# Performance work log

Hardware: AMD Instinct MI355X
Metric: run time of the kernel (lower is better)

## Reference

```python
import jax, jax.numpy as jnp
import numpy as np
import math

H = 16
D_MODEL = 1024
D_K = D_MODEL // H  # 64
B = 4
S = 2048
D_V = 64


def setup_inputs() -> dict:
    key0 = jax.random.key(0)
    ks = jax.random.split(key0, 7)
    scale = 1.0 / math.sqrt(D_MODEL)
    return {
        "query": jax.random.normal(ks[0], (B, S, D_MODEL), jnp.float32),
        "key": jax.random.normal(ks[1], (B, S, D_MODEL), jnp.float32),
        "value": jax.random.normal(ks[2], (B, D_V, S), jnp.float32),
        "Wq": jax.random.normal(ks[3], (D_MODEL, D_MODEL), jnp.float32) * scale,
        "bq": jax.random.normal(ks[4], (D_MODEL,), jnp.float32) * scale,
        "Wk": jax.random.normal(ks[5], (D_MODEL, D_MODEL), jnp.float32) * scale,
        "bk": jax.random.normal(ks[6], (D_MODEL,), jnp.float32) * scale,
    }


def reference(query, key, value, Wq, bq, Wk, bk):
    nb = query.shape[0]
    # Linear projections then split heads: [B,S,d_model] -> [B,h,S,d_k]
    q = (query @ Wq.T + bq).reshape(nb, -1, H, D_K).transpose(0, 2, 1, 3)
    k = (key @ Wk.T + bk).reshape(nb, -1, H, D_K).transpose(0, 2, 1, 3)
    # value.repeat(h,1,1,1).permute(1,0,3,2): [B,dv,Sk] -> broadcast over heads
    # with last two axes swapped -> effectively v[b,s,d] = value[b,d,s]
    v = jnp.swapaxes(value, 1, 2)  # [B, Sk, dv]
    # Scaled dot-product attention (mask branch is a no-op: m == zeros)
    scores = jnp.einsum("bhqd,bhkd->bhqk", q, k) / math.sqrt(D_K)
    p_attn = jax.nn.softmax(scores, axis=-1)
    # value identical across heads, contract directly with base v
    x = jnp.einsum("bhqk,bkd->bhqd", p_attn, v)  # [B,h,Sq,dv]
    return (jnp.mean(x, axis=1), q)
```

## Files before the change

### kernel.cpp

```cpp
#include <hip/hip_runtime.h>


typedef unsigned short u16;
typedef __attribute__((ext_vector_type(8))) u16 u16x8;
typedef __attribute__((ext_vector_type(8))) __bf16 bf16x8;
typedef __attribute__((ext_vector_type(4))) float f32x4;
typedef __attribute__((ext_vector_type(16))) float f32x16;
typedef __attribute__((ext_vector_type(2))) unsigned u32x2;
typedef __attribute__((ext_vector_type(4))) unsigned u32x4;

typedef const __attribute__((address_space(1))) void gvoid;
typedef __attribute__((address_space(3))) void lvoid;

__device__ __forceinline__ void gload16(const void* g, void* l) {
  __builtin_amdgcn_global_load_lds((gvoid*)g, (lvoid*)l, 16, 0, 0);
}

__device__ __forceinline__ u16 f2bf(float f) {
  unsigned u = __builtin_bit_cast(unsigned, f);
  u += 0x7fffu + ((u >> 16) & 1u);
  return (u16)(u >> 16);
}

__device__ __forceinline__ unsigned cvtpk(float lo, float hi) {
  unsigned r;
  asm("v_cvt_pk_bf16_f32 %0, %1, %2" : "=v"(r) : "v"(lo), "v"(hi));
  return r;
}

__device__ __forceinline__ float exp2a(float x) {
  float r;
  asm("v_exp_f32 %0, %1" : "=v"(r) : "v"(x));
  return r;
}

__device__ __forceinline__ f32x16 zero16() {
  f32x16 z;
#pragma unroll
  for (int i = 0; i < 16; ++i) z[i] = 0.f;
  return z;
}

__global__ void cvt_small(const float* __restrict__ wq, const float* __restrict__ wk,
                          const float* __restrict__ v,
                          u16* __restrict__ wqb, u16* __restrict__ wkb, u16* __restrict__ vb) {
  int i = blockIdx.x * 256 + threadIdx.x;
  const float* s;
  u16* d;
  int off;
  if (i < 262144)      { s = wq; d = wqb; off = i; }
  else if (i < 524288) { s = wk; d = wkb; off = i - 262144; }
  else if (i < 655360) { s = v;  d = vb;  off = i - 524288; }
  else return;
  float4 x = reinterpret_cast<const float4*>(s)[off];
  ushort4 o;
  o.x = f2bf(x.x); o.y = f2bf(x.y); o.z = f2bf(x.z); o.w = f2bf(x.w);
  reinterpret_cast<ushort4*>(d)[off] = o;
}

__global__ __launch_bounds__(256) void proj_gemm(
    const float* __restrict__ qf, const float* __restrict__ kf,
    const u16* __restrict__ Wqb, const u16* __restrict__ Wkb,
    const float* __restrict__ bq, const float* __restrict__ bk,
    float* __restrict__ out1, u16* __restrict__ k_ws)
{
  const int z = blockIdx.z;
  const float* __restrict__ A = z ? kf : qf;
  const u16* __restrict__ W = z ? Wkb : Wqb;
  const float* __restrict__ bias = z ? bk : bq;

  __shared__ u16 As[128 * 64];
  __shared__ u16 Bs[128 * 64];

  const int tid = threadIdx.x;
  const int lane = tid & 63;
  const int w = tid >> 6;
  const int ln = lane & 15;
  const int lh = lane >> 4;
  const int wm = w >> 1, wn = w & 1;
  const int n0 = blockIdx.x * 128;
  const int j0 = blockIdx.y * 128;

  f32x4 acc[4][4];
#pragma unroll
  for (int mt = 0; mt < 4; ++mt)
#pragma unroll
    for (int nt = 0; nt < 4; ++nt)
      acc[mt][nt] = f32x4{0.f, 0.f, 0.f, 0.f};

  const int r_ = tid >> 3, c8_ = tid & 7;

  for (int kt = 0; kt < 16; ++kt) {
    __syncthreads();
#pragma unroll
    for (int it = 0; it < 4; ++it) {
      int r = it * 32 + r_;
      gload16(&W[(size_t)(j0 + r) * 1024 + kt * 64 + c8_ * 8], &Bs[(it * 256 + w * 64) * 8]);
    }
#pragma unroll
    for (int j = 0; j < 4; ++j) {
      int u = tid + j * 256;
      int r = u >> 3, c8 = (u & 7) * 8;
      const float* s = &A[(size_t)(n0 + r) * 1024 + kt * 64 + c8];
      float4 x0 = *reinterpret_cast<const float4*>(s);
      float4 x1 = *reinterpret_cast<const float4*>(s + 4);
      u32x4 wv{cvtpk(x0.x, x0.y), cvtpk(x0.z, x0.w), cvtpk(x1.x, x1.y), cvtpk(x1.z, x1.w)};
      *reinterpret_cast<u32x4*>(&As[r * 64 + c8]) = wv;
    }
    __syncthreads();
#pragma unroll
    for (int ks = 0; ks < 2; ++ks) {
      bf16x8 a[4], bfr[4];
#pragma unroll
      for (int mt = 0; mt < 4; ++mt)
        a[mt] = __builtin_bit_cast(bf16x8,
            *reinterpret_cast<const u16x8*>(&As[(wm * 64 + mt * 16 + ln) * 64 + lh * 8 + ks * 32]));
#pragma unroll
      for (int nt = 0; nt < 4; ++nt)
        bfr[nt] = __builtin_bit_cast(bf16x8,
            *reinterpret_cast<const u16x8*>(&Bs[(wn * 64 + nt * 16 + ln) * 64 + lh * 8 + ks * 32]));
      __builtin_amdgcn_s_setprio(1);
#pragma unroll
      for (int mt = 0; mt < 4; ++mt)
#pragma unroll
        for (int nt = 0; nt < 4; ++nt)
          acc[mt][nt] = __builtin_amdgcn_mfma_f32_16x16x32_bf16(a[mt], bfr[nt], acc[mt][nt], 0, 0, 0);
      __builtin_amdgcn_s_setprio(0);
    }
  }

#pragma unroll
  for (int nt = 0; nt < 4; ++nt) {
    int j = j0 + wn * 64 + nt * 16 + ln;
    float bv = bias[j];
    int h = j >> 6, d = j & 63;
#pragma unroll
    for (int mt = 0; mt < 4; ++mt) {
#pragma unroll
      for (int r = 0; r < 4; ++r) {
        int n = n0 + wm * 64 + mt * 16 + lh * 4 + r;
        int bidx = n >> 11, s = n & 2047;
        size_t off = ((size_t)(bidx * 16 + h) * 2048 + s) * 64 + d;
        float val = acc[mt][nt][r] + bv;
        if (z == 0) out1[off] = val;
        else        k_ws[off] = f2bf(val);
      }
    }
  }
}

#define SOFTMAX_CVT(P, PF0, PF1, LACC)                                               \
  {                                                                                  \
    _Pragma("unroll")                                                                \
    for (int r = 0; r < 16; ++r) P[r] = exp2a(P[r]);                                 \
    LACC += (((P[0]+P[1])+(P[2]+P[3])) + ((P[4]+P[5])+(P[6]+P[7])))                  \
          + (((P[8]+P[9])+(P[10]+P[11])) + ((P[12]+P[13])+(P[14]+P[15])));           \
    u32x2 sA0 = __builtin_amdgcn_permlane32_swap(cvtpk(P[0],P[1]),   cvtpk(P[4],P[5]),   false,false); \
    u32x2 sB0 = __builtin_amdgcn_permlane32_swap(cvtpk(P[2],P[3]),   cvtpk(P[6],P[7]),   false,false); \
    u32x2 sA1 = __builtin_amdgcn_permlane32_swap(cvtpk(P[8],P[9]),   cvtpk(P[12],P[13]), false,false); \
    u32x2 sB1 = __builtin_amdgcn_permlane32_swap(cvtpk(P[10],P[11]), cvtpk(P[14],P[15]), false,false); \
    u32x4 w0_{sA0[0], sB0[0], sA0[1], sB0[1]};                                       \
    u32x4 w1_{sA1[0], sB1[0], sA1[1], sB1[1]};                                       \
    PF0 = __builtin_bit_cast(bf16x8, w0_);                                           \
    PF1 = __builtin_bit_cast(bf16x8, w1_);                                           \
  }

#define ST_BLOCK(ST)                                                                 \
  {                                                                                  \
    f32x16 pA = zero16(), pB = zero16();                                             \
    __builtin_amdgcn_s_setprio(1);                                                   \
    _Pragma("unroll")                                                                \
    for (int c = 0; c < 4; ++c) {                                                    \
      int ka = bo + ((((ST * 32 + l31) * 128) + c * 32 + hi * 16) ^ xm);             \
      bf16x8 kf = __builtin_bit_cast(bf16x8, *reinterpret_cast<const u16x8*>(KtB + ka)); \
      pA = __builtin_amdgcn_mfma_f32_32x32x16_bf16(kf, aqA[c], pA, 0, 0, 0);         \
      pB = __builtin_amdgcn_mfma_f32_32x32x16_bf16(kf, aqB[c], pB, 0, 0, 0);         \
    }                                                                                \
    __builtin_amdgcn_s_setprio(0);                                                   \
    bf16x8 fA0, fA1, fB0, fB1;                                                       \
    SOFTMAX_CVT(pA, fA0, fA1, lA);                                                   \
    SOFTMAX_CVT(pB, fB0, fB1, lB);                                                   \
    _Pragma("unroll")                                                                \
    for (int kc = 0; kc < 2; ++kc) {                                                 \
      int cb = ST * 64 + kc * 32 + hi * 16;                                          \
      bf16x8 vA = __builtin_bit_cast(bf16x8,                                         \
          *reinterpret_cast<const u16x8*>(VtB + bo + ((l31 * 128 + cb) ^ xm)));      \
      bf16x8 vB = __builtin_bit_cast(bf16x8,                                         \
          *reinterpret_cast<const u16x8*>(VtB + bo + (((32 + l31) * 128 + cb) ^ xm))); \
      bf16x8 fA = kc ? fA1 : fA0;                                                    \
      bf16x8 fB = kc ? fB1 : fB0;                                                    \
      __builtin_amdgcn_s_setprio(1);                                                 \
      oA0 = __builtin_amdgcn_mfma_f32_32x32x16_bf16(vA, fA, oA0, 0, 0, 0);           \
      oB0 = __builtin_amdgcn_mfma_f32_32x32x16_bf16(vB, fA, oB0, 0, 0, 0);           \
      oA1 = __builtin_amdgcn_mfma_f32_32x32x16_bf16(vA, fB, oA1, 0, 0, 0);           \
      oB1 = __builtin_amdgcn_mfma_f32_32x32x16_bf16(vB, fB, oB1, 0, 0, 0);           \
      __builtin_amdgcn_s_setprio(0);                                                 \
    }                                                                                \
  }

__global__ __launch_bounds__(256) void attn_kernel(
    const float* __restrict__ qf, const u16* __restrict__ k_ws,
    const u16* __restrict__ valb, u16* __restrict__ x_ws)
{
  const int wgid = (blockIdx.x & 7) * 64 + (blockIdx.x >> 3);
  const int qblk = wgid & 7;
  const int h = (wgid >> 3) & 15;
  const int b = wgid >> 7;
  const int bh = b * 16 + h;

  const int tid = threadIdx.x, lane = tid & 63, w = tid >> 6;
  const int l31 = lane & 31, hi = lane >> 5;
  const int xm = (lane & 7) << 4;

  __shared__ u16 Kt[2][4096];
  __shared__ u16 Vt[2][4096];
  char* KtB = (char*)&Kt[0][0];
  char* VtB = (char*)&Vt[0][0];

  bf16x8 aqA[4], aqB[4];
  {
    const float qs = 0.125f * 1.4426950408889634f;
    const size_t qb0 = ((size_t)bh * 2048 + qblk * 256 + w * 64 + l31) * 64;
    const size_t qb1 = qb0 + (size_t)32 * 64;
#pragma unroll
    for (int c = 0; c < 4; ++c) {
#pragma unroll
      for (int g = 0; g < 2; ++g) {
        const float* src = g ? &qf[qb1 + c * 16 + hi * 8] : &qf[qb0 + c * 16 + hi * 8];
        float4 v0 = *reinterpret_cast<const float4*>(src);
        float4 v1 = *reinterpret_cast<const float4*>(src + 4);
        u16x8 t;
        t[0] = f2bf(v0.x * qs); t[1] = f2bf(v0.y * qs);
        t[2] = f2bf(v0.z * qs); t[3] = f2bf(v0.w * qs);
        t[4] = f2bf(v1.x * qs); t[5] = f2bf(v1.y * qs);
        t[6] = f2bf(v1.z * qs); t[7] = f2bf(v1.w * qs);
        if (g) aqB[c] = __builtin_bit_cast(bf16x8, t);
        else   aqA[c] = __builtin_bit_cast(bf16x8, t);
      }
    }
  }

  const u16* kg = k_ws + (size_t)bh * 131072;
  const u16* vg = valb + (size_t)b * 131072;
  const int u0 = tid, u1 = tid + 256;
  const u16* ks0 = kg + (u0 >> 3) * 64 + ((u0 ^ (u0 >> 3)) & 7) * 8;
  const u16* ks1 = kg + (u1 >> 3) * 64 + ((u1 ^ (u1 >> 3)) & 7) * 8;
  const u16* vs0 = vg + (u0 >> 3) * 2048 + ((u0 ^ (u0 >> 3)) & 7) * 8;
  const u16* vs1 = vg + (u1 >> 3) * 2048 + ((u1 ^ (u1 >> 3)) & 7) * 8;
  u16* kd0 = &Kt[0][(w * 64) * 8];
  u16* kd1 = &Kt[0][(256 + w * 64) * 8];
  u16* vd0 = &Vt[0][(w * 64) * 8];
  u16* vd1 = &Vt[0][(256 + w * 64) * 8];

  gload16(ks0, kd0); gload16(ks1, kd1);
  gload16(vs0, vd0); gload16(vs1, vd1);

  float lA = 0.0f, lB = 0.0f;
  f32x16 oA0 = zero16(), oB0 = zero16(), oA1 = zero16(), oB1 = zero16();
  int cur = 0;
  __syncthreads();

  for (int t = 0; t < 32; ++t) {
    if (t < 31) {
      int nb = (cur ^ 1) * 4096;
      size_t ko = (size_t)(t + 1) * 4096;
      int vo = (t + 1) * 64;
      gload16(ks0 + ko, kd0 + nb); gload16(ks1 + ko, kd1 + nb);
      gload16(vs0 + vo, vd0 + nb); gload16(vs1 + vo, vd1 + nb);
    }
    const int bo = cur * 8192;

    ST_BLOCK(0)
    ST_BLOCK(1)

    __syncthreads();
    cur ^= 1;
  }

  float lrA = lA + __shfl_xor(lA, 32);
  float lrB = lB + __shfl_xor(lB, 32);
  float invA = 1.0f / lrA, invB = 1.0f / lrB;
  size_t ob0 = ((size_t)bh * 2048 + qblk * 256 + w * 64 + l31) * 64;
  size_t ob1 = ob0 + (size_t)32 * 64;
#pragma unroll
  for (int g = 0; g < 4; ++g) {
    u32x2 aa{cvtpk(oA0[g*4+0]*invA, oA0[g*4+1]*invA), cvtpk(oA0[g*4+2]*invA, oA0[g*4+3]*invA)};
    u32x2 bb{cvtpk(oB0[g*4+0]*invA, oB0[g*4+1]*invA), cvtpk(oB0[g*4+2]*invA, oB0[g*4+3]*invA)};
    u32x2 cc{cvtpk(oA1[g*4+0]*invB, oA1[g*4+1]*invB), cvtpk(oA1[g*4+2]*invB, oA1[g*4+3]*invB)};
    u32x2 dd{cvtpk(oB1[g*4+0]*invB, oB1[g*4+1]*invB), cvtpk(oB1[g*4+2]*invB, oB1[g*4+3]*invB)};
    *reinterpret_cast<u32x2*>(&x_ws[ob0 + g * 8 + hi * 4]) = aa;
    *reinterpret_cast<u32x2*>(&x_ws[ob0 + 32 + g * 8 + hi * 4]) = bb;
    *reinterpret_cast<u32x2*>(&x_ws[ob1 + g * 8 + hi * 4]) = cc;
    *reinterpret_cast<u32x2*>(&x_ws[ob1 + 32 + g * 8 + hi * 4]) = dd;
  }
}

__global__ void mean_heads(const u16* __restrict__ x_ws, float* __restrict__ out0) {
  int i = blockIdx.x * 256 + threadIdx.x;
  int d0 = (i & 7) * 8;
  int s = (i >> 3) & 2047;
  int b = i >> 14;
  float acc[8];
#pragma unroll
  for (int j = 0; j < 8; ++j) acc[j] = 0.f;
#pragma unroll
  for (int h = 0; h < 16; ++h) {
    u16x8 v = *reinterpret_cast<const u16x8*>(
        &x_ws[(((size_t)(b * 16 + h) * 2048 + s) << 6) + d0]);
#pragma unroll
    for (int j = 0; j < 8; ++j)
      acc[j] += __builtin_bit_cast(float, (unsigned)v[j] << 16);
  }
  float4 o0{acc[0] * 0.0625f, acc[1] * 0.0625f, acc[2] * 0.0625f, acc[3] * 0.0625f};
  float4 o1{acc[4] * 0.0625f, acc[5] * 0.0625f, acc[6] * 0.0625f, acc[7] * 0.0625f};
  size_t ob = ((size_t)(b * 2048 + s) << 6) + d0;
  *reinterpret_cast<float4*>(&out0[ob]) = o0;
  *reinterpret_cast<float4*>(&out0[ob + 4]) = o1;
}

extern "C" void kernel_launch(void* const* d_in, const int* in_sizes, int n_in,
                              void* d_out, int out_size, void* d_ws, size_t ws_size,
                              hipStream_t stream) {
  (void)in_sizes; (void)n_in; (void)out_size; (void)ws_size;
  const float* query = (const float*)d_in[0];
  const float* key   = (const float*)d_in[1];
  const float* value = (const float*)d_in[2];
  const float* Wq    = (const float*)d_in[3];
  const float* bq    = (const float*)d_in[4];
  const float* Wk    = (const float*)d_in[5];
  const float* bk    = (const float*)d_in[6];

  float* out0 = (float*)d_out;
  float* out1 = out0 + 524288;

  char* ws = (char*)d_ws;
  const size_t MB = 1u << 20;
  u16* Wqb  = (u16*)(ws + 32 * MB);
  u16* Wkb  = (u16*)(ws + 34 * MB);
  u16* valb = (u16*)(ws + 36 * MB);
  u16* k_ws = (u16*)(ws + 37 * MB);
  u16* x_ws = (u16*)(ws + 0);

  cvt_small<<<2560, 256, 0, stream>>>(Wq, Wk, value, Wqb, Wkb, valb);
  proj_gemm<<<dim3(64, 8, 2), 256, 0, stream>>>(query, key, Wqb, Wkb, bq, bk, out1, k_ws);
  attn_kernel<<<512, 256, 0, stream>>>(out1, k_ws, valb, x_ws);
  mean_heads<<<256, 256, 0, stream>>>(x_ws, out0);
}
```

Measured before the change: 164.0 us.

## Double-buffer projection GEMM tiles and triple-buffer attention K/V loads

The projection GEMM gets double-buffered LDS. The next K-tile's weight loads and activation reads are issued before the MFMA loop, and the bf16 conversion and store happen afterward, so only one barrier is needed per iteration. The attention kernel moves from two to three K/V LDS buffers, prefetching two tiles ahead with explicit vmcnt waits and raw s_barrier in place of __syncthreads. This aims to hide global-load latency behind compute, at the cost of more LDS (which may reduce occupancy) and more registers for the staged activations.

```diff
diff --git a/kernel.cpp b/kernel.cpp
--- a/kernel.cpp
+++ b/kernel.cpp
@@ -69,8 +69,8 @@
   const u16* __restrict__ W = z ? Wkb : Wqb;
   const float* __restrict__ bias = z ? bk : bq;
 
-  __shared__ u16 As[128 * 64];
-  __shared__ u16 Bs[128 * 64];
+  __shared__ u16 As[2][128 * 64];
+  __shared__ u16 Bs[2][128 * 64];
 
   const int tid = threadIdx.x;
   const int lane = tid & 63;
@@ -90,35 +90,53 @@
 
   const int r_ = tid >> 3, c8_ = tid & 7;
 
+#pragma unroll
+  for (int it = 0; it < 4; ++it) {
+    int r = it * 32 + r_;
+    gload16(&W[(size_t)(j0 + r) * 1024 + c8_ * 8], &Bs[0][(it * 256 + w * 64) * 8]);
+  }
+#pragma unroll
+  for (int j = 0; j < 4; ++j) {
+    int u = tid + j * 256;
+    int r = u >> 3, c8 = (u & 7) * 8;
+    const float* s = &A[(size_t)(n0 + r) * 1024 + c8];
+    float4 x0 = *reinterpret_cast<const float4*>(s);
+    float4 x1 = *reinterpret_cast<const float4*>(s + 4);
+    u32x4 wv{cvtpk(x0.x, x0.y), cvtpk(x0.z, x0.w), cvtpk(x1.x, x1.y), cvtpk(x1.z, x1.w)};
+    *reinterpret_cast<u32x4*>(&As[0][r * 64 + c8]) = wv;
+  }
+  __syncthreads();
+
   for (int kt = 0; kt < 16; ++kt) {
-    __syncthreads();
-#pragma unroll
-    for (int it = 0; it < 4; ++it) {
-      int r = it * 32 + r_;
-      gload16(&W[(size_t)(j0 + r) * 1024 + kt * 64 + c8_ * 8], &Bs[(it * 256 + w * 64) * 8]);
-    }
-#pragma unroll
-    for (int j = 0; j < 4; ++j) {
-      int u = tid + j * 256;
-      int r = u >> 3, c8 = (u & 7) * 8;
-      const float* s = &A[(size_t)(n0 + r) * 1024 + kt * 64 + c8];
-      float4 x0 = *reinterpret_cast<const float4*>(s);
-      float4 x1 = *reinterpret_cast<const float4*>(s + 4);
-      u32x4 wv{cvtpk(x0.x, x0.y), cvtpk(x0.z, x0.w), cvtpk(x1.x, x1.y), cvtpk(x1.z, x1.w)};
-      *reinterpret_cast<u32x4*>(&As[r * 64 + c8]) = wv;
-    }
-    __syncthreads();
+    const int cur = kt & 1, nb = cur ^ 1;
+    float4 ax0[4], ax1[4];
+    if (kt < 15) {
+#pragma unroll
+      for (int it = 0; it < 4; ++it) {
+        int r = it * 32 + r_;
+        gload16(&W[(size_t)(j0 + r) * 1024 + (kt + 1) * 64 + c8_ * 8],
+                &Bs[nb][(it * 256 + w * 64) * 8]);
+      }
+#pragma unroll
+      for (int j = 0; j < 4; ++j) {
+        int u = tid + j * 256;
+        int r = u >> 3, c8 = (u & 7) * 8;
+        const float* s = &A[(size_t)(n0 + r) * 1024 + (kt + 1) * 64 + c8];
+        ax0[j] = *reinterpret_cast<const float4*>(s);
+        ax1[j] = *reinterpret_cast<const float4*>(s + 4);
+      }
+    }
 #pragma unroll
     for (int ks = 0; ks < 2; ++ks) {
       bf16x8 a[4], bfr[4];
 #pragma unroll
       for (int mt = 0; mt < 4; ++mt)
         a[mt] = __builtin_bit_cast(bf16x8,
-            *reinterpret_cast<const u16x8*>(&As[(wm * 64 + mt * 16 + ln) * 64 + lh * 8 + ks * 32]));
+            *reinterpret_cast<const u16x8*>(&As[cur][(wm * 64 + mt * 16 + ln) * 64 + lh * 8 + ks * 32]));
 #pragma unroll
       for (int nt = 0; nt < 4; ++nt)
         bfr[nt] = __builtin_bit_cast(bf16x8,
-            *reinterpret_cast<const u16x8*>(&Bs[(wn * 64 + nt * 16 + ln) * 64 + lh * 8 + ks * 32]));
+            *reinterpret_cast<const u16x8*>(&Bs[cur][(wn * 64 + nt * 16 + ln) * 64 + lh * 8 + ks * 32]));
       __builtin_amdgcn_s_setprio(1);
 #pragma unroll
       for (int mt = 0; mt < 4; ++mt)
@@ -126,6 +144,17 @@
         for (int nt = 0; nt < 4; ++nt)
           acc[mt][nt] = __builtin_amdgcn_mfma_f32_16x16x32_bf16(a[mt], bfr[nt], acc[mt][nt], 0, 0, 0);
       __builtin_amdgcn_s_setprio(0);
+    }
+    if (kt < 15) {
+#pragma unroll
+      for (int j = 0; j < 4; ++j) {
+        int u = tid + j * 256;
+        int r = u >> 3, c8 = (u & 7) * 8;
+        u32x4 wv{cvtpk(ax0[j].x, ax0[j].y), cvtpk(ax0[j].z, ax0[j].w),
+                 cvtpk(ax1[j].x, ax1[j].y), cvtpk(ax1[j].z, ax1[j].w)};
+        *reinterpret_cast<u32x4*>(&As[nb][r * 64 + c8]) = wv;
+      }
+      __syncthreads();
     }
   }
 
@@ -212,8 +241,8 @@
   const int l31 = lane & 31, hi = lane >> 5;
   const int xm = (lane & 7) << 4;
 
-  __shared__ u16 Kt[2][4096];
-  __shared__ u16 Vt[2][4096];
+  __shared__ u16 Kt[3][4096];
+  __shared__ u16 Vt[3][4096];
   char* KtB = (char*)&Kt[0][0];
   char* VtB = (char*)&Vt[0][0];
 
@@ -239,6 +268,7 @@
       }
     }
   }
+  __builtin_amdgcn_sched_barrier(0);
 
   const u16* kg = k_ws + (size_t)bh * 131072;
   const u16* vg = valb + (size_t)b * 131072;
@@ -247,34 +277,47 @@
   const u16* ks1 = kg + (u1 >> 3) * 64 + ((u1 ^ (u1 >> 3)) & 7) * 8;
   const u16* vs0 = vg + (u0 >> 3) * 2048 + ((u0 ^ (u0 >> 3)) & 7) * 8;
   const u16* vs1 = vg + (u1 >> 3) * 2048 + ((u1 ^ (u1 >> 3)) & 7) * 8;
-  u16* kd0 = &Kt[0][(w * 64) * 8];
-  u16* kd1 = &Kt[0][(256 + w * 64) * 8];
-  u16* vd0 = &Vt[0][(w * 64) * 8];
-  u16* vd1 = &Vt[0][(256 + w * 64) * 8];
-
-  gload16(ks0, kd0); gload16(ks1, kd1);
-  gload16(vs0, vd0); gload16(vs1, vd1);
+  char* kb0 = (char*)Kt + w * 1024;
+  char* kb1 = (char*)Kt + 4096 + w * 1024;
+  char* vb0 = (char*)Vt + w * 1024;
+  char* vb1 = (char*)Vt + 4096 + w * 1024;
+
+  gload16(ks0, kb0);          gload16(ks1, kb1);
+  gload16(vs0, vb0);          gload16(vs1, vb1);
+  gload16(ks0 + 4096, kb0 + 8192); gload16(ks1 + 4096, kb1 + 8192);
+  gload16(vs0 + 64,   vb0 + 8192); gload16(vs1 + 64,   vb1 + 8192);
 
   float lA = 0.0f, lB = 0.0f;
   f32x16 oA0 = zero16(), oB0 = zero16(), oA1 = zero16(), oB1 = zero16();
+
+  asm volatile("s_waitcnt vmcnt(4)" ::: "memory");
+  __builtin_amdgcn_sched_barrier(0);
+  __builtin_amdgcn_s_barrier();
+  __builtin_amdgcn_sched_barrier(0);
+
   int cur = 0;
-  __syncthreads();
-
   for (int t = 0; t < 32; ++t) {
-    if (t < 31) {
-      int nb = (cur ^ 1) * 4096;
-      size_t ko = (size_t)(t + 1) * 4096;
-      int vo = (t + 1) * 64;
-      gload16(ks0 + ko, kd0 + nb); gload16(ks1 + ko, kd1 + nb);
-      gload16(vs0 + vo, vd0 + nb); gload16(vs1 + vo, vd1 + nb);
-    }
-    const int bo = cur * 8192;
+    const int bo = cur;
 
     ST_BLOCK(0)
     ST_BLOCK(1)
 
-    __syncthreads();
-    cur ^= 1;
+    if (t < 30) {
+      int so = cur + 16384; if (so >= 24576) so -= 24576;
+      size_t ko = (size_t)(t + 2) * 4096;
+      int vo = (t + 2) * 64;
+      gload16(ks0 + ko, kb0 + so); gload16(ks1 + ko, kb1 + so);
+      gload16(vs0 + vo, vb0 + so); gload16(vs1 + vo, vb1 + so);
+      asm volatile("s_waitcnt vmcnt(4)" ::: "memory");
+    } else if (t == 30) {
+      asm volatile("s_waitcnt vmcnt(0)" ::: "memory");
+    }
+    if (t < 31) {
+      __builtin_amdgcn_sched_barrier(0);
+      __builtin_amdgcn_s_barrier();
+      __builtin_amdgcn_sched_barrier(0);
+    }
+    cur += 8192; if (cur == 24576) cur = 0;
   }
 
   float lrA = lA + __shfl_xor(lA, 32);
```

Measured after the change: 176.6 us. 7.7% more time.

## Split attention KV range across two blocks and double-buffer projection GEMM

Applied to the files above, without the earlier changes.

The attention kernel now splits each query block's key/value range into two halves handled by separate workgroups, doubling the grid. Each half writes unnormalized bf16 partial outputs and row sums to workspace, and mean_heads merges the halves and normalizes before averaging over heads. The intent is more parallelism and better CU occupancy, at the cost of twice the intermediate output traffic. Separately, the projection GEMM gets double-buffered shared memory, so the next tile's loads overlap the current tile's MFMAs. The new row-sum buffer reuses workspace that held the converted Wq, which is safe only because that buffer is dead by the time attention runs.

```diff
diff --git a/kernel.cpp b/kernel.cpp
--- a/kernel.cpp
+++ b/kernel.cpp
@@ -69,8 +69,8 @@
   const u16* __restrict__ W = z ? Wkb : Wqb;
   const float* __restrict__ bias = z ? bk : bq;
 
-  __shared__ u16 As[128 * 64];
-  __shared__ u16 Bs[128 * 64];
+  __shared__ u16 As[2][128 * 64];
+  __shared__ u16 Bs[2][128 * 64];
 
   const int tid = threadIdx.x;
   const int lane = tid & 63;
@@ -90,35 +90,53 @@
 
   const int r_ = tid >> 3, c8_ = tid & 7;
 
+#pragma unroll
+  for (int it = 0; it < 4; ++it) {
+    int r = it * 32 + r_;
+    gload16(&W[(size_t)(j0 + r) * 1024 + c8_ * 8], &Bs[0][(it * 256 + w * 64) * 8]);
+  }
+#pragma unroll
+  for (int j = 0; j < 4; ++j) {
+    int u = tid + j * 256;
+    int r = u >> 3, c8 = (u & 7) * 8;
+    const float* s = &A[(size_t)(n0 + r) * 1024 + c8];
+    float4 x0 = *reinterpret_cast<const float4*>(s);
+    float4 x1 = *reinterpret_cast<const float4*>(s + 4);
+    u32x4 wv{cvtpk(x0.x, x0.y), cvtpk(x0.z, x0.w), cvtpk(x1.x, x1.y), cvtpk(x1.z, x1.w)};
+    *reinterpret_cast<u32x4*>(&As[0][r * 64 + c8]) = wv;
+  }
+  __syncthreads();
+
   for (int kt = 0; kt < 16; ++kt) {
-    __syncthreads();
-#pragma unroll
-    for (int it = 0; it < 4; ++it) {
-      int r = it * 32 + r_;
-      gload16(&W[(size_t)(j0 + r) * 1024 + kt * 64 + c8_ * 8], &Bs[(it * 256 + w * 64) * 8]);
-    }
-#pragma unroll
-    for (int j = 0; j < 4; ++j) {
-      int u = tid + j * 256;
-      int r = u >> 3, c8 = (u & 7) * 8;
-      const float* s = &A[(size_t)(n0 + r) * 1024 + kt * 64 + c8];
-      float4 x0 = *reinterpret_cast<const float4*>(s);
-      float4 x1 = *reinterpret_cast<const float4*>(s + 4);
-      u32x4 wv{cvtpk(x0.x, x0.y), cvtpk(x0.z, x0.w), cvtpk(x1.x, x1.y), cvtpk(x1.z, x1.w)};
-      *reinterpret_cast<u32x4*>(&As[r * 64 + c8]) = wv;
-    }
-    __syncthreads();
+    const int cur = kt & 1, nb = cur ^ 1;
+    float4 ax0[4], ax1[4];
+    if (kt < 15) {
+#pragma unroll
+      for (int it = 0; it < 4; ++it) {
+        int r = it * 32 + r_;
+        gload16(&W[(size_t)(j0 + r) * 1024 + (kt + 1) * 64 + c8_ * 8],
+                &Bs[nb][(it * 256 + w * 64) * 8]);
+      }
+#pragma unroll
+      for (int j = 0; j < 4; ++j) {
+        int u = tid + j * 256;
+        int r = u >> 3, c8 = (u & 7) * 8;
+        const float* s = &A[(size_t)(n0 + r) * 1024 + (kt + 1) * 64 + c8];
+        ax0[j] = *reinterpret_cast<const float4*>(s);
+        ax1[j] = *reinterpret_cast<const float4*>(s + 4);
+      }
+    }
 #pragma unroll
     for (int ks = 0; ks < 2; ++ks) {
       bf16x8 a[4], bfr[4];
 #pragma unroll
       for (int mt = 0; mt < 4; ++mt)
         a[mt] = __builtin_bit_cast(bf16x8,
-            *reinterpret_cast<const u16x8*>(&As[(wm * 64 + mt * 16 + ln) * 64 + lh * 8 + ks * 32]));
+            *reinterpret_cast<const u16x8*>(&As[cur][(wm * 64 + mt * 16 + ln) * 64 + lh * 8 + ks * 32]));
 #pragma unroll
       for (int nt = 0; nt < 4; ++nt)
         bfr[nt] = __builtin_bit_cast(bf16x8,
-            *reinterpret_cast<const u16x8*>(&Bs[(wn * 64 + nt * 16 + ln) * 64 + lh * 8 + ks * 32]));
+            *reinterpret_cast<const u16x8*>(&Bs[cur][(wn * 64 + nt * 16 + ln) * 64 + lh * 8 + ks * 32]));
       __builtin_amdgcn_s_setprio(1);
 #pragma unroll
       for (int mt = 0; mt < 4; ++mt)
@@ -126,6 +144,17 @@
         for (int nt = 0; nt < 4; ++nt)
           acc[mt][nt] = __builtin_amdgcn_mfma_f32_16x16x32_bf16(a[mt], bfr[nt], acc[mt][nt], 0, 0, 0);
       __builtin_amdgcn_s_setprio(0);
+    }
+    if (kt < 15) {
+#pragma unroll
+      for (int j = 0; j < 4; ++j) {
+        int u = tid + j * 256;
+        int r = u >> 3, c8 = (u & 7) * 8;
+        u32x4 wv{cvtpk(ax0[j].x, ax0[j].y), cvtpk(ax0[j].z, ax0[j].w),
+                 cvtpk(ax1[j].x, ax1[j].y), cvtpk(ax1[j].z, ax1[j].w)};
+        *reinterpret_cast<u32x4*>(&As[nb][r * 64 + c8]) = wv;
+      }
+      __syncthreads();
     }
   }
 
@@ -198,14 +227,15 @@
     }                                                                                \
   }
 
-__global__ __launch_bounds__(256) void attn_kernel(
+__global__ __launch_bounds__(256, 4) void attn_kernel(
     const float* __restrict__ qf, const u16* __restrict__ k_ws,
-    const u16* __restrict__ valb, u16* __restrict__ x_ws)
+    const u16* __restrict__ valb, u16* __restrict__ x_ws, float* __restrict__ l_ws)
 {
-  const int wgid = (blockIdx.x & 7) * 64 + (blockIdx.x >> 3);
-  const int qblk = wgid & 7;
-  const int h = (wgid >> 3) & 15;
-  const int b = wgid >> 7;
+  const int wgid = (blockIdx.x & 7) * 128 + (blockIdx.x >> 3);
+  const int kvh = wgid & 1;
+  const int qblk = (wgid >> 1) & 7;
+  const int h = (wgid >> 4) & 15;
+  const int b = wgid >> 8;
   const int bh = b * 16 + h;
 
   const int tid = threadIdx.x, lane = tid & 63, w = tid >> 6;
@@ -240,8 +270,8 @@
     }
   }
 
-  const u16* kg = k_ws + (size_t)bh * 131072;
-  const u16* vg = valb + (size_t)b * 131072;
+  const u16* kg = k_ws + (size_t)bh * 131072 + (size_t)kvh * 65536;
+  const u16* vg = valb + (size_t)b * 131072 + kvh * 1024;
   const int u0 = tid, u1 = tid + 256;
   const u16* ks0 = kg + (u0 >> 3) * 64 + ((u0 ^ (u0 >> 3)) & 7) * 8;
   const u16* ks1 = kg + (u1 >> 3) * 64 + ((u1 ^ (u1 >> 3)) & 7) * 8;
@@ -260,8 +290,8 @@
   int cur = 0;
   __syncthreads();
 
-  for (int t = 0; t < 32; ++t) {
-    if (t < 31) {
+  for (int t = 0; t < 16; ++t) {
+    if (t < 15) {
       int nb = (cur ^ 1) * 4096;
       size_t ko = (size_t)(t + 1) * 4096;
       int vo = (t + 1) * 64;
@@ -279,15 +309,19 @@
 
   float lrA = lA + __shfl_xor(lA, 32);
   float lrB = lB + __shfl_xor(lB, 32);
-  float invA = 1.0f / lrA, invB = 1.0f / lrB;
-  size_t ob0 = ((size_t)bh * 2048 + qblk * 256 + w * 64 + l31) * 64;
+  int qbase = qblk * 256 + w * 64 + l31;
+  if (hi == 0) {
+    l_ws[kvh * 131072 + bh * 2048 + qbase] = lrA;
+    l_ws[kvh * 131072 + bh * 2048 + qbase + 32] = lrB;
+  }
+  size_t ob0 = ((size_t)kvh << 23) + (((size_t)bh * 2048 + qbase) << 6);
   size_t ob1 = ob0 + (size_t)32 * 64;
 #pragma unroll
   for (int g = 0; g < 4; ++g) {
-    u32x2 aa{cvtpk(oA0[g*4+0]*invA, oA0[g*4+1]*invA), cvtpk(oA0[g*4+2]*invA, oA0[g*4+3]*invA)};
-    u32x2 bb{cvtpk(oB0[g*4+0]*invA, oB0[g*4+1]*invA), cvtpk(oB0[g*4+2]*invA, oB0[g*4+3]*invA)};
-    u32x2 cc{cvtpk(oA1[g*4+0]*invB, oA1[g*4+1]*invB), cvtpk(oA1[g*4+2]*invB, oA1[g*4+3]*invB)};
-    u32x2 dd{cvtpk(oB1[g*4+0]*invB, oB1[g*4+1]*invB), cvtpk(oB1[g*4+2]*invB, oB1[g*4+3]*invB)};
+    u32x2 aa{cvtpk(oA0[g*4+0], oA0[g*4+1]), cvtpk(oA0[g*4+2], oA0[g*4+3])};
+    u32x2 bb{cvtpk(oB0[g*4+0], oB0[g*4+1]), cvtpk(oB0[g*4+2], oB0[g*4+3])};
+    u32x2 cc{cvtpk(oA1[g*4+0], oA1[g*4+1]), cvtpk(oA1[g*4+2], oA1[g*4+3])};
+    u32x2 dd{cvtpk(oB1[g*4+0], oB1[g*4+1]), cvtpk(oB1[g*4+2], oB1[g*4+3])};
     *reinterpret_cast<u32x2*>(&x_ws[ob0 + g * 8 + hi * 4]) = aa;
     *reinterpret_cast<u32x2*>(&x_ws[ob0 + 32 + g * 8 + hi * 4]) = bb;
     *reinterpret_cast<u32x2*>(&x_ws[ob1 + g * 8 + hi * 4]) = cc;
@@ -295,7 +329,8 @@
   }
 }
 
-__global__ void mean_heads(const u16* __restrict__ x_ws, float* __restrict__ out0) {
+__global__ void mean_heads(const u16* __restrict__ x_ws, const float* __restrict__ l_ws,
+                           float* __restrict__ out0) {
   int i = blockIdx.x * 256 + threadIdx.x;
   int d0 = (i & 7) * 8;
   int s = (i >> 3) & 2047;
@@ -305,17 +340,21 @@
   for (int j = 0; j < 8; ++j) acc[j] = 0.f;
 #pragma unroll
   for (int h = 0; h < 16; ++h) {
-    u16x8 v = *reinterpret_cast<const u16x8*>(
-        &x_ws[(((size_t)(b * 16 + h) * 2048 + s) << 6) + d0]);
+    int bh = b * 16 + h;
+    size_t o0 = (((size_t)bh * 2048 + s) << 6) + d0;
+    u16x8 v0 = *reinterpret_cast<const u16x8*>(&x_ws[o0]);
+    u16x8 v1 = *reinterpret_cast<const u16x8*>(&x_ws[((size_t)1 << 23) + o0]);
+    float inv = 1.0f / (l_ws[bh * 2048 + s] + l_ws[131072 + bh * 2048 + s]);
 #pragma unroll
     for (int j = 0; j < 8; ++j)
-      acc[j] += __builtin_bit_cast(float, (unsigned)v[j] << 16);
-  }
-  float4 o0{acc[0] * 0.0625f, acc[1] * 0.0625f, acc[2] * 0.0625f, acc[3] * 0.0625f};
-  float4 o1{acc[4] * 0.0625f, acc[5] * 0.0625f, acc[6] * 0.0625f, acc[7] * 0.0625f};
+      acc[j] += (__builtin_bit_cast(float, (unsigned)v0[j] << 16) +
+                 __builtin_bit_cast(float, (unsigned)v1[j] << 16)) * inv;
+  }
+  float4 o0v{acc[0] * 0.0625f, acc[1] * 0.0625f, acc[2] * 0.0625f, acc[3] * 0.0625f};
+  float4 o1v{acc[4] * 0.0625f, acc[5] * 0.0625f, acc[6] * 0.0625f, acc[7] * 0.0625f};
   size_t ob = ((size_t)(b * 2048 + s) << 6) + d0;
-  *reinterpret_cast<float4*>(&out0[ob]) = o0;
-  *reinterpret_cast<float4*>(&out0[ob + 4]) = o1;
+  *reinterpret_cast<float4*>(&out0[ob]) = o0v;
+  *reinterpret_cast<float4*>(&out0[ob + 4]) = o1v;
 }
 
 extern "C" void kernel_launch(void* const* d_in, const int* in_sizes, int n_in,
@@ -335,14 +374,15 @@
 
   char* ws = (char*)d_ws;
   const size_t MB = 1u << 20;
+  u16* x_ws  = (u16*)(ws + 0);
+  float* l_ws = (float*)(ws + 32 * MB);
   u16* Wqb  = (u16*)(ws + 32 * MB);
   u16* Wkb  = (u16*)(ws + 34 * MB);
   u16* valb = (u16*)(ws + 36 * MB);
   u16* k_ws = (u16*)(ws + 37 * MB);
-  u16* x_ws = (u16*)(ws + 0);
 
   cvt_small<<<2560, 256, 0, stream>>>(Wq, Wk, value, Wqb, Wkb, valb);
   proj_gemm<<<dim3(64, 8, 2), 256, 0, stream>>>(query, key, Wqb, Wkb, bq, bk, out1, k_ws);
-  attn_kernel<<<512, 256, 0, stream>>>(out1, k_ws, valb, x_ws);
-  mean_heads<<<256, 256, 0, stream>>>(x_ws, out0);
-}
+  attn_kernel<<<1024, 256, 0, stream>>>(out1, k_ws, valb, x_ws, l_ws);
+  mean_heads<<<256, 256, 0, stream>>>(x_ws, l_ws, out0);
+}
```

Result: slower. 656.0 us (+299.9%).
